# Optimization experiments

Measured on AMD Instinct MI355X. Metric: run time of the kernel, lower is better.

Reference implementation:

```python
import jax, jax.numpy as jnp
import numpy as np

SIZE = 256  # matrix dimension n; input vector length = n*(n-1)/2
BATCH = 512

# strictly-lower indices in the same row-major (i, j<i) order as the module's l_indices
_ROWS, _COLS = np.tril_indices(SIZE, k=-1)


def setup_inputs() -> dict:
    key = jax.random.key(0)
    m = SIZE * (SIZE - 1) // 2
    # z entries are partial-correlation-like values, must lie in (-1, 1)
    vec = jax.random.uniform(key, (BATCH, m), dtype=jnp.float32, minval=-0.99, maxval=0.99)
    return {"vec": vec}


def reference(vec):
    B = vec.shape[0]
    n = SIZE
    # scatter vector into strictly-lower triangle: (B, n, n)
    z = jnp.zeros((B, n, n), dtype=vec.dtype).at[:, _ROWS, _COLS].set(vec)
    signs = jnp.sign(z)
    signs = jnp.where(signs == 0, jnp.asarray(1.0, vec.dtype), signs)
    z2 = z * z

    row_idx = jnp.arange(n)  # (n,)

    def step(rowsum, inp):
        # rowsum: (B, n) running sum of x_squared over already-built columns, per row
        j, z2_col = inp  # z2_col: (B, n) = z^2[:, :, j]
        base = z2_col * (1.0 - rowsum)           # lower entries (rows > j)
        col = jnp.where(row_idx[None, :] == j, jnp.asarray(1.0, vec.dtype),
                        jnp.where(row_idx[None, :] < j, jnp.asarray(0.0, vec.dtype), base))
        return rowsum + col, col

    z2_cols = jnp.moveaxis(z2, -1, 0)  # (n_col, B, n_row)
    _, x2_cols = jax.lax.scan(step, jnp.zeros((B, n), dtype=vec.dtype),
                              (jnp.arange(n), z2_cols))
    # x2_cols: (n_col, B, n_row) -> (B, n_row, n_col)
    x2 = jnp.moveaxis(x2_cols, 0, -1)
    return jnp.sqrt(x2) * signs
```

## Files before the change

kernel.cpp:

```cpp
#include <hip/hip_runtime.h>


#define SIZE 256
#define BATCH 512
#define M (SIZE * (SIZE - 1) / 2)

template <int CTRL, int ROW_MASK>
__device__ __forceinline__ float scan_mul(float p) {
    int shifted = __builtin_amdgcn_update_dpp(
        __builtin_bit_cast(int, 1.0f),
        __builtin_bit_cast(int, p),
        CTRL, ROW_MASK, 0xF, false);
    return p * __builtin_bit_cast(float, shifted);
}

__global__ __launch_bounds__(256) void chol_from_z_kernel(
    const float* __restrict__ vec, float* __restrict__ out) {
    const int lane = threadIdx.x & 63;
    const int wave = (blockIdx.x * blockDim.x + threadIdx.x) >> 6;
    const int b = wave >> 8;
    const int i = wave & 255;

    const size_t row_off = (size_t)b * M + (size_t)((i * (i - 1)) >> 1);
    const float* __restrict__ s = vec + row_off;
    float* __restrict__ dst = out + (((size_t)b << 8) + (size_t)i) * SIZE;

    const int L = i;
    const int j0 = lane << 2;

    const float z0 = (j0     < L) ? s[j0]     : 0.f;
    const float z1 = (j0 + 1 < L) ? s[j0 + 1] : 0.f;
    const float z2 = (j0 + 2 < L) ? s[j0 + 2] : 0.f;
    const float z3 = (j0 + 3 < L) ? s[j0 + 3] : 0.f;

    const float t0 = 1.f - z0 * z0;
    const float t1 = 1.f - z1 * z1;
    const float t2 = 1.f - z2 * z2;
    const float t3 = 1.f - z3 * z3;

    float p = (t0 * t1) * (t2 * t3);

    p = scan_mul<0x111, 0xF>(p);
    p = scan_mul<0x112, 0xF>(p);
    p = scan_mul<0x114, 0xF>(p);
    p = scan_mul<0x118, 0xF>(p);
    p = scan_mul<0x142, 0xA>(p);
    p = scan_mul<0x143, 0xC>(p);

    float run = __shfl_up(p, 1, 64);
    if (lane == 0) run = 1.f;

    float4 o;
    o.x = (j0     < L) ? z0 * sqrtf(run) : ((j0     == i) ? 1.f : 0.f); run *= t0;
    o.y = (j0 + 1 < L) ? z1 * sqrtf(run) : ((j0 + 1 == i) ? 1.f : 0.f); run *= t1;
    o.z = (j0 + 2 < L) ? z2 * sqrtf(run) : ((j0 + 2 == i) ? 1.f : 0.f); run *= t2;
    o.w = (j0 + 3 < L) ? z3 * sqrtf(run) : ((j0 + 3 == i) ? 1.f : 0.f);

    *(float4*)(dst + j0) = o;
}

extern "C" void kernel_launch(void* const* d_in, const int* in_sizes, int n_in,
                              void* d_out, int out_size, void* d_ws, size_t ws_size,
                              hipStream_t stream) {
    const float* vec = (const float*)d_in[0];
    float* out = (float*)d_out;
    const int n_waves = BATCH * SIZE;
    const int blocks = n_waves / 4;
    chol_from_z_kernel<<<blocks, 256, 0, stream>>>(vec, out);
}
```

Measured before the change: 180.8 us.

## Specialize per-row element count by row length and use DPP exclusive shift

Rows shorter than 64 or 128 elements are handled with 1 or 2 elements per lane, and the trailing known-zero region is written directly as zeros. Loads become unconditional, reading past the row into the next row's data (clamped only at the end of the buffer) and masking afterwards, which removes load predication. The shfl_up used for the exclusive scan is replaced by a DPP wave shift, and the wave index is made scalar with readfirstlane. The aim is to cut instructions on short rows; in exchange the code has three template paths and extra loads of unneeded data.

```diff
diff --git a/kernel.cpp b/kernel.cpp
--- a/kernel.cpp
+++ b/kernel.cpp
@@ -4,42 +4,47 @@
 #define SIZE 256
 #define BATCH 512
 #define M (SIZE * (SIZE - 1) / 2)
+#define TOTAL (BATCH * M)
 
 template <int CTRL, int ROW_MASK>
 __device__ __forceinline__ float scan_mul(float p) {
-    int shifted = __builtin_amdgcn_update_dpp(
+    int sh = __builtin_amdgcn_update_dpp(
         __builtin_bit_cast(int, 1.0f),
         __builtin_bit_cast(int, p),
         CTRL, ROW_MASK, 0xF, false);
-    return p * __builtin_bit_cast(float, shifted);
+    return p * __builtin_bit_cast(float, sh);
 }
 
-__global__ __launch_bounds__(256) void chol_from_z_kernel(
-    const float* __restrict__ vec, float* __restrict__ out) {
-    const int lane = threadIdx.x & 63;
-    const int wave = (blockIdx.x * blockDim.x + threadIdx.x) >> 6;
-    const int b = wave >> 8;
-    const int i = wave & 255;
+__device__ __forceinline__ float excl_shift_one(float p) {
+    int r = __builtin_amdgcn_update_dpp(
+        __builtin_bit_cast(int, 1.0f),
+        __builtin_bit_cast(int, p),
+        0x138 , 0xF, 0xF, false);
+    return __builtin_bit_cast(float, r);
+}
 
-    const size_t row_off = (size_t)b * M + (size_t)((i * (i - 1)) >> 1);
-    const float* __restrict__ s = vec + row_off;
-    float* __restrict__ dst = out + (((size_t)b << 8) + (size_t)i) * SIZE;
+template <int C>
+__device__ __forceinline__ void do_row(const float* __restrict__ s,
+                                       float* __restrict__ dst,
+                                       const int i, const int lane,
+                                       const int maxidx) {
+    const int j0 = lane * C;
 
-    const int L = i;
-    const int j0 = lane << 2;
+    float z[C], t[C];
+    #pragma unroll
+    for (int e = 0; e < C; ++e) {
+        int idx = j0 + e;
+        if (C == 4 && e == 3) idx = (idx < maxidx) ? idx : maxidx;
+        const float raw = s[idx];
+        z[e] = (j0 < i - e) ? raw : 0.f;
+        t[e] = 1.f - z[e] * z[e];
+    }
 
-    const float z0 = (j0     < L) ? s[j0]     : 0.f;
-    const float z1 = (j0 + 1 < L) ? s[j0 + 1] : 0.f;
-    const float z2 = (j0 + 2 < L) ? s[j0 + 2] : 0.f;
-    const float z3 = (j0 + 3 < L) ? s[j0 + 3] : 0.f;
+    float local = t[0];
+    #pragma unroll
+    for (int e = 1; e < C; ++e) local *= t[e];
 
-    const float t0 = 1.f - z0 * z0;
-    const float t1 = 1.f - z1 * z1;
-    const float t2 = 1.f - z2 * z2;
-    const float t3 = 1.f - z3 * z3;
-
-    float p = (t0 * t1) * (t2 * t3);
-
+    float p = local;
     p = scan_mul<0x111, 0xF>(p);
     p = scan_mul<0x112, 0xF>(p);
     p = scan_mul<0x114, 0xF>(p);
@@ -47,16 +52,45 @@
     p = scan_mul<0x142, 0xA>(p);
     p = scan_mul<0x143, 0xC>(p);
 
-    float run = __shfl_up(p, 1, 64);
-    if (lane == 0) run = 1.f;
+    float run = excl_shift_one(p);
 
-    float4 o;
-    o.x = (j0     < L) ? z0 * sqrtf(run) : ((j0     == i) ? 1.f : 0.f); run *= t0;
-    o.y = (j0 + 1 < L) ? z1 * sqrtf(run) : ((j0 + 1 == i) ? 1.f : 0.f); run *= t1;
-    o.z = (j0 + 2 < L) ? z2 * sqrtf(run) : ((j0 + 2 == i) ? 1.f : 0.f); run *= t2;
-    o.w = (j0 + 3 < L) ? z3 * sqrtf(run) : ((j0 + 3 == i) ? 1.f : 0.f);
+    float o[C];
+    #pragma unroll
+    for (int e = 0; e < C; ++e) {
+        const float v = z[e] * sqrtf(run);
+        o[e] = (j0 == i - e) ? 1.f : v;
+        run *= t[e];
+    }
 
-    *(float4*)(dst + j0) = o;
+    if (C == 4) {
+        *(float4*)(dst + j0) = make_float4(o[0], o[1], o[2], o[3]);
+    } else if (C == 2) {
+        *(float2*)(dst + j0) = make_float2(o[0], o[1]);
+        *(float2*)(dst + 128 + j0) = make_float2(0.f, 0.f);
+    } else {
+        dst[j0] = o[0];
+        dst[64 + j0] = 0.f;
+        dst[128 + j0] = 0.f;
+        dst[192 + j0] = 0.f;
+    }
+}
+
+__global__ __launch_bounds__(256) void chol_from_z_kernel(
+    const float* __restrict__ vec, float* __restrict__ out) {
+    const int lane = threadIdx.x & 63;
+    const int wib = __builtin_amdgcn_readfirstlane((int)threadIdx.x >> 6);
+    const int wave = (int)blockIdx.x * 4 + wib;
+    const int b = wave >> 8;
+    const int i = wave & 255;
+
+    const int row_off = b * M + ((i * (i - 1)) >> 1);
+    const float* __restrict__ s = vec + row_off;
+    float* __restrict__ dst = out + ((size_t)wave << 8);
+    const int maxidx = (TOTAL - 1) - row_off;
+
+    if (i < 64)        do_row<1>(s, dst, i, lane, maxidx);
+    else if (i < 128)  do_row<2>(s, dst, i, lane, maxidx);
+    else               do_row<4>(s, dst, i, lane, maxidx);
 }
 
 extern "C" void kernel_launch(void* const* d_in, const int* in_sizes, int n_in,
```

Result: faster. 176.2 us (-2.6%).
